# Kernel tuning notes

Hardware: AMD Instinct MI355X
Metric: run time of the kernel (lower is better)

## Reference

```python
import jax, jax.numpy as jnp
import numpy as np

B, S, HS = 2, 2048, 2048
H, KVH, D = 8, 1, 256
ROPE_BASE = 10000.0


def _rope_cos_sin(position_ids, dim, base=ROPE_BASE):
    # position_ids: (B, S) int -> cos/sin: (B, S, dim)
    inv_freq = 1.0 / (base ** (jnp.arange(0, dim, 2, dtype=jnp.float32) / dim))
    thetas = position_ids.astype(jnp.float32)[..., None] * inv_freq  # (B,S,dim/2)
    emb = jnp.concatenate([thetas, thetas], axis=-1)  # (B,S,dim)
    return jnp.cos(emb), jnp.sin(emb)


def _rotate_half(x):
    x1, x2 = jnp.split(x, 2, axis=-1)
    return jnp.concatenate([-x2, x1], axis=-1)


def _apply_rope(q, k, cos, sin):
    # q,k: (B,h,S,D); cos,sin: (B,S,D) -> unsqueeze head dim
    cos = cos[:, None, :, :]
    sin = sin[:, None, :, :]
    q_emb = q * cos + _rotate_half(q) * sin
    k_emb = k * cos + _rotate_half(k) * sin
    return q_emb, k_emb


def setup_inputs() -> dict:
    key = jax.random.key(0)
    k0, k1, k2, k3, k4 = jax.random.split(key, 5)
    hidden_states = jax.random.normal(k0, (B, S, HS), jnp.float32)
    # causal additive mask: 0 where j<=i, large negative otherwise
    causal = jnp.tril(jnp.ones((S, S), dtype=bool))
    attention_mask = jnp.where(causal, 0.0, -1e9).astype(jnp.float32)
    attention_mask = jnp.broadcast_to(attention_mask[None, None], (B, 1, S, S))
    position_ids = jnp.broadcast_to(jnp.arange(S, dtype=jnp.int32)[None], (B, S))
    scale = 0.02
    Wq = jax.random.normal(k1, (HS, H * D), jnp.float32) * scale
    Wk = jax.random.normal(k2, (HS, KVH * D), jnp.float32) * scale
    Wv = jax.random.normal(k3, (HS, KVH * D), jnp.float32) * scale
    Wo = jax.random.normal(k4, (H * D, HS), jnp.float32) * scale
    return {"hidden_states": hidden_states, "attention_mask": attention_mask,
            "position_ids": position_ids, "Wq": Wq, "Wk": Wk, "Wv": Wv, "Wo": Wo}


def reference(hidden_states, attention_mask, position_ids, Wq, Wk, Wv, Wo):
    bs, seq_len, _ = hidden_states.shape
    q = (hidden_states @ Wq).reshape(bs, seq_len, H, D).transpose(0, 2, 1, 3)     # (B,H,S,D)
    k = (hidden_states @ Wk).reshape(bs, seq_len, KVH, D).transpose(0, 2, 1, 3)   # (B,KVH,S,D)
    v = (hidden_states @ Wv).reshape(bs, seq_len, KVH, D).transpose(0, 2, 1, 3)
    cos, sin = _rope_cos_sin(position_ids, D)
    q, k = _apply_rope(q, k, cos, sin)
    n_rep = H // KVH
    k = jnp.repeat(k, n_rep, axis=1)  # GQA repeat -> (B,H,S,D)
    v = jnp.repeat(v, n_rep, axis=1)
    scores = jnp.einsum('bhqd,bhkd->bhqk', q, k) / jnp.sqrt(jnp.float32(D))
    scores = scores + attention_mask
    attn = jax.nn.softmax(scores.astype(jnp.float32), axis=-1).astype(q.dtype)
    out = jnp.einsum('bhqk,bhkd->bhqd', attn, v)            # (B,H,S,D)
    out = out.transpose(0, 2, 1, 3).reshape(bs, seq_len, H * D)
    return out @ Wo
```

## Files before the change

### kernel.cpp

```cpp
#include <hip/hip_runtime.h>
#include <hip/hip_bf16.h>

typedef __bf16 bf16x8 __attribute__((ext_vector_type(8)));
typedef __bf16 bf16x4 __attribute__((ext_vector_type(4)));
typedef float  f32x4  __attribute__((ext_vector_type(4)));

#define MFMA16(a, b, c) __builtin_amdgcn_mfma_f32_16x16x32_bf16((a), (b), (c), 0, 0, 0)

#define GLOBAL_AS(p) ((const __attribute__((address_space(1))) void*)(p))
#define LDS_AS(p)    ((__attribute__((address_space(3))) void*)(p))

static __device__ __forceinline__ void tr64(const float* __restrict__ W,
                                            __bf16* __restrict__ Bt,
                                            int K, int N, int n0, int k0,
                                            int tid, float (*t)[69])
{
    const int rk = tid >> 4, rc = (tid & 15) * 4;
#pragma unroll
    for (int p = 0; p < 4; ++p) {
        f32x4 v = *(const f32x4*)&W[(size_t)(k0 + p * 16 + rk) * N + n0 + rc];
        t[p * 16 + rk][rc + 0] = v[0];
        t[p * 16 + rk][rc + 1] = v[1];
        t[p * 16 + rk][rc + 2] = v[2];
        t[p * 16 + rk][rc + 3] = v[3];
    }
    __syncthreads();
    const int wn = tid >> 3, wk = (tid & 7) * 8;
#pragma unroll
    for (int p = 0; p < 2; ++p) {
        bf16x8 o;
#pragma unroll
        for (int j = 0; j < 8; ++j)
            o[j] = (__bf16)t[wk + j][p * 32 + wn];
        *(bf16x8*)&Bt[(size_t)(n0 + p * 32 + wn) * K + k0 + wk] = o;
    }
}

__global__ __launch_bounds__(256) void prep_kernel(const float* __restrict__ hidden,
                                                   __bf16* __restrict__ hb,
                                                   float2* __restrict__ cs,
                                                   const float* __restrict__ Wq,
                                                   const float* __restrict__ Wk,
                                                   const float* __restrict__ Wv,
                                                   const float* __restrict__ Wo,
                                                   __bf16* __restrict__ Wqkvt,
                                                   __bf16* __restrict__ Wot)
{
    __shared__ float tf[64][69];
    const int bx = blockIdx.x;
    const int tid = threadIdx.x;

    if (bx < 4096) {
        const int idx = bx * 256 + tid;
        const float4* p = (const float4*)hidden + (size_t)idx * 2;
        float4 a = p[0], b = p[1];
        bf16x8 o;
        o[0] = (__bf16)a.x; o[1] = (__bf16)a.y; o[2] = (__bf16)a.z; o[3] = (__bf16)a.w;
        o[4] = (__bf16)b.x; o[5] = (__bf16)b.y; o[6] = (__bf16)b.z; o[7] = (__bf16)b.w;
        ((bf16x8*)hb)[idx] = o;
    } else if (bx < 5120) {
        const int gid = (bx - 4096) * 256 + tid;
        const int s = gid >> 7, i = gid & 127;
        const float theta = (float)s * exp2f((float)i * (-13.287712379549449f / 128.f));
        float sn, c;
        sincosf(theta, &sn, &c);
        cs[s * 128 + i] = make_float2(c, sn);
    } else if (bx < 6144) {
        const int bidx = bx - 5120;
        tr64(Wq, Wqkvt, 2048, 2048, (bidx & 31) * 64, (bidx >> 5) * 64, tid, tf);
    } else if (bx < 6272) {
        const int bidx = bx - 6144;
        tr64(Wk, Wqkvt + (size_t)2048 * 2048, 2048, 256,
             (bidx & 3) * 64, (bidx >> 2) * 64, tid, tf);
    } else if (bx < 6400) {
        const int bidx = bx - 6272;
        tr64(Wv, Wqkvt + (size_t)2304 * 2048, 2048, 256,
             (bidx & 3) * 64, (bidx >> 2) * 64, tid, tf);
    } else {
        const int bidx = bx - 6400;
        tr64(Wo, Wot, 2048, 2048, (bidx & 31) * 64, (bidx >> 5) * 64, tid, tf);
    }
}

__global__ __launch_bounds__(256) void postq_kernel(__bf16* __restrict__ qkv,
                                                    const float2* __restrict__ cs,
                                                    __bf16* __restrict__ vT)
{
    __shared__ __bf16 tb[32][33];
    const int bx = blockIdx.x;
    const int t = threadIdx.x;

    if (bx < 4096) {
        const int bs = bx;
        const int s = bs & 2047;
        const float QS = 0.09016843787599907f;

        const int hh = t >> 5, i0 = (t & 31) * 4;
        float2 c0 = cs[s * 128 + i0 + 0], c1 = cs[s * 128 + i0 + 1];
        float2 c2 = cs[s * 128 + i0 + 2], c3 = cs[s * 128 + i0 + 3];
        {
            __bf16* p = qkv + (size_t)bs * 2560 + hh * 256 + i0;
            bf16x4 x1 = *(const bf16x4*)p;
            bf16x4 x2 = *(const bf16x4*)(p + 128);
            bf16x4 o1, o2;
            o1[0] = (__bf16)(((float)x1[0] * c0.x - (float)x2[0] * c0.y) * QS);
            o2[0] = (__bf16)(((float)x2[0] * c0.x + (float)x1[0] * c0.y) * QS);
            o1[1] = (__bf16)(((float)x1[1] * c1.x - (float)x2[1] * c1.y) * QS);
            o2[1] = (__bf16)(((float)x2[1] * c1.x + (float)x1[1] * c1.y) * QS);
            o1[2] = (__bf16)(((float)x1[2] * c2.x - (float)x2[2] * c2.y) * QS);
            o2[2] = (__bf16)(((float)x2[2] * c2.x + (float)x1[2] * c2.y) * QS);
            o1[3] = (__bf16)(((float)x1[3] * c3.x - (float)x2[3] * c3.y) * QS);
            o2[3] = (__bf16)(((float)x2[3] * c3.x + (float)x1[3] * c3.y) * QS);
            *(bf16x4*)p = o1;
            *(bf16x4*)(p + 128) = o2;
        }
        if (t < 32) {
            const int j0 = t * 4;
            float2 d0 = cs[s * 128 + j0 + 0], d1 = cs[s * 128 + j0 + 1];
            float2 d2 = cs[s * 128 + j0 + 2], d3 = cs[s * 128 + j0 + 3];
            __bf16* p = qkv + (size_t)bs * 2560 + 2048 + j0;
            bf16x4 x1 = *(const bf16x4*)p;
            bf16x4 x2 = *(const bf16x4*)(p + 128);
            bf16x4 o1, o2;
            o1[0] = (__bf16)((float)x1[0] * d0.x - (float)x2[0] * d0.y);
            o2[0] = (__bf16)((float)x2[0] * d0.x + (float)x1[0] * d0.y);
            o1[1] = (__bf16)((float)x1[1] * d1.x - (float)x2[1] * d1.y);
            o2[1] = (__bf16)((float)x2[1] * d1.x + (float)x1[1] * d1.y);
            o1[2] = (__bf16)((float)x1[2] * d2.x - (float)x2[2] * d2.y);
            o2[2] = (__bf16)((float)x2[2] * d2.x + (float)x1[2] * d2.y);
            o1[3] = (__bf16)((float)x1[3] * d3.x - (float)x2[3] * d3.y);
            o2[3] = (__bf16)((float)x2[3] * d3.x + (float)x1[3] * d3.y);
            *(bf16x4*)p = o1;
            *(bf16x4*)(p + 128) = o2;
        }
    } else {
        const int bidx = bx - 4096;
        const int s0 = (bidx & 63) * 32;
        const int d0 = ((bidx >> 6) & 7) * 32;
        const int b  = bidx >> 9;
        const int x = t & 31, y = t >> 5;
#pragma unroll
        for (int r = 0; r < 4; ++r)
            tb[y + r * 8][x] = qkv[(size_t)(b * 2048 + s0 + y + r * 8) * 2560 + 2304 + d0 + x];
        __syncthreads();
#pragma unroll
        for (int r = 0; r < 4; ++r)
            vT[(size_t)(b * 256 + d0 + y + r * 8) * 2048 + s0 + x] = tb[x][y + r * 8];
    }
}

template <typename TC>
__global__ __launch_bounds__(512, 2) void gemm_mp(const __bf16* __restrict__ A,
                                                  const __bf16* __restrict__ Bt,
                                                  TC* __restrict__ C,
                                                  int M, int N, int K)
{
    __shared__ __bf16 As[3][128 * 64];
    __shared__ __bf16 Bs[3][256 * 64];

    const int tid  = threadIdx.x;
    const int wave = tid >> 6, lane = tid & 63;
    const int quad = lane >> 4, l16 = lane & 15;
    const int wm = (wave >> 2) * 64, wn = (wave & 3) * 64;
    const int bm = blockIdx.y * 128, bn = blockIdx.x * 256;
    const int xk = l16 & 7;

    const int srow = tid >> 3;
    const int schk = (tid & 7) ^ (srow & 7);
    const __bf16* gA[2];
    const __bf16* gB[4];
#pragma unroll
    for (int p = 0; p < 2; ++p)
        gA[p] = A + (size_t)(bm + p * 64 + srow) * K + schk * 8;
#pragma unroll
    for (int p = 0; p < 4; ++p)
        gB[p] = Bt + (size_t)(bn + p * 64 + srow) * K + schk * 8;

#define STAGE_A2(s, t) do {                                                       \
    const size_t ko_ = (size_t)(t) * 64;                                          \
    __builtin_amdgcn_global_load_lds(GLOBAL_AS(gA[0] + ko_),                      \
        LDS_AS((char*)As[s] + tid * 16), 16, 0, 0);                               \
    __builtin_amdgcn_global_load_lds(GLOBAL_AS(gA[1] + ko_),                      \
        LDS_AS((char*)As[s] + 8192 + tid * 16), 16, 0, 0);                        \
} while (0)
#define STAGE_B01(s, t) do {                                                      \
    const size_t ko_ = (size_t)(t) * 64;                                          \
    __builtin_amdgcn_global_load_lds(GLOBAL_AS(gB[0] + ko_),                      \
        LDS_AS((char*)Bs[s] + tid * 16), 16, 0, 0);                               \
    __builtin_amdgcn_global_load_lds(GLOBAL_AS(gB[1] + ko_),                      \
        LDS_AS((char*)Bs[s] + 8192 + tid * 16), 16, 0, 0);                        \
} while (0)
#define STAGE_B23(s, t) do {                                                      \
    const size_t ko_ = (size_t)(t) * 64;                                          \
    __builtin_amdgcn_global_load_lds(GLOBAL_AS(gB[2] + ko_),                      \
        LDS_AS((char*)Bs[s] + 16384 + tid * 16), 16, 0, 0);                       \
    __builtin_amdgcn_global_load_lds(GLOBAL_AS(gB[3] + ko_),                      \
        LDS_AS((char*)Bs[s] + 24576 + tid * 16), 16, 0, 0);                       \
} while (0)

    f32x4 acc[4][4] = {};
    const int nk = K >> 6;

    STAGE_A2(0, 0); STAGE_B01(0, 0); STAGE_B23(0, 0);
    STAGE_A2(1, 1); STAGE_B01(1, 1); STAGE_B23(1, 1);
    asm volatile("s_waitcnt vmcnt(6)" ::: "memory");
    __builtin_amdgcn_s_barrier();

    int s = 0;
    for (int t = 0; t < nk; ++t) {
        const int sp = (s + 2 >= 3) ? s - 1 : s + 2;
        const bool more2 = (t + 2 < nk);
        const bool more1 = (t + 1 < nk);

        bf16x8 af[4][2], bfr[2][2];
#pragma unroll
        for (int mi = 0; mi < 4; ++mi)
#pragma unroll
            for (int kh = 0; kh < 2; ++kh)
                af[mi][kh] = *(const bf16x8*)
                    &As[s][(wm + mi * 16 + l16) * 64 + (((kh << 2) | quad) ^ xk) * 8];
#pragma unroll
        for (int ni = 0; ni < 2; ++ni)
#pragma unroll
            for (int kh = 0; kh < 2; ++kh)
                bfr[ni][kh] = *(const bf16x8*)
                    &Bs[s][(wn + ni * 16 + l16) * 64 + (((kh << 2) | quad) ^ xk) * 8];
        if (more2) { STAGE_A2(sp, t + 2); STAGE_B01(sp, t + 2); }
        __builtin_amdgcn_sched_barrier(0);
        __builtin_amdgcn_s_barrier();
        asm volatile("s_waitcnt lgkmcnt(0)" ::: "memory");
        __builtin_amdgcn_sched_barrier(0);
        __builtin_amdgcn_s_setprio(1);
#pragma unroll
        for (int ni = 0; ni < 2; ++ni)
#pragma unroll
            for (int mi = 0; mi < 4; ++mi) {
                acc[mi][ni] = MFMA16(af[mi][0], bfr[ni][0], acc[mi][ni]);
                acc[mi][ni] = MFMA16(af[mi][1], bfr[ni][1], acc[mi][ni]);
            }
        __builtin_amdgcn_s_setprio(0);
        __builtin_amdgcn_sched_barrier(0);
        __builtin_amdgcn_s_barrier();

        bf16x8 bf2[2][2];
#pragma unroll
        for (int ni = 0; ni < 2; ++ni)
#pragma unroll
            for (int kh = 0; kh < 2; ++kh)
                bf2[ni][kh] = *(const bf16x8*)
                    &Bs[s][(wn + (2 + ni) * 16 + l16) * 64 + (((kh << 2) | quad) ^ xk) * 8];
        if (more2) STAGE_B23(sp, t + 2);
        __builtin_amdgcn_sched_barrier(0);
        __builtin_amdgcn_s_barrier();
        asm volatile("s_waitcnt lgkmcnt(0)" ::: "memory");
        __builtin_amdgcn_sched_barrier(0);
        __builtin_amdgcn_s_setprio(1);
#pragma unroll
        for (int ni = 0; ni < 2; ++ni)
#pragma unroll
            for (int mi = 0; mi < 4; ++mi) {
                acc[mi][2 + ni] = MFMA16(af[mi][0], bf2[ni][0], acc[mi][2 + ni]);
                acc[mi][2 + ni] = MFMA16(af[mi][1], bf2[ni][1], acc[mi][2 + ni]);
            }
        __builtin_amdgcn_s_setprio(0);
        if (more1) {
            if (more2) asm volatile("s_waitcnt vmcnt(6)" ::: "memory");
            else       asm volatile("s_waitcnt vmcnt(0)" ::: "memory");
        }
        __builtin_amdgcn_sched_barrier(0);
        __builtin_amdgcn_s_barrier();
        s = (s + 1 == 3) ? 0 : s + 1;
    }
#undef STAGE_A2
#undef STAGE_B01
#undef STAGE_B23

#pragma unroll
    for (int mi = 0; mi < 4; ++mi)
#pragma unroll
        for (int ni = 0; ni < 4; ++ni)
#pragma unroll
            for (int r = 0; r < 4; ++r) {
                int row = bm + wm + mi * 16 + quad * 4 + r;
                int col = bn + wn + ni * 16 + l16;
                C[(size_t)row * N + col] = (TC)acc[mi][ni][r];
            }
}

static __device__ __forceinline__ void stage8(const __bf16* src, __bf16* dst,
                                              size_t src_step)
{
#pragma unroll
    for (int p = 0; p < 8; ++p)
        __builtin_amdgcn_global_load_lds(GLOBAL_AS(src + (size_t)p * src_step),
                                         LDS_AS(dst + p * 2048), 16, 0, 0);
}

__global__ __launch_bounds__(256, 2) void attn_kernel(const __bf16* __restrict__ qkv,
                                                      const __bf16* __restrict__ vTg,
                                                      __bf16* __restrict__ og)
{
    __shared__ __bf16 Ks[64 * 256];
    __shared__ __bf16 Vs[256 * 64];
    __shared__ __bf16 Ps[4][32][36];

    const int b = blockIdx.z, h = blockIdx.y;
    const int xx = (int)blockIdx.x;
    const int half = xx >> 1;
    const bool rev = ((xx & 1) == 0) ^ (b != 0);
    const int qt = rev ? 31 - half : half;
    const int q0 = qt * 64;
    const int tid  = threadIdx.x;
    const int wave = tid >> 6, lane = tid & 63;
    const int quad = lane >> 4, l16 = lane & 15;
    const int xork = l16 & 7;
    const int wm2 = wave >> 1, wn2 = wave & 1;

    bf16x8 onef;
#pragma unroll
    for (int e = 0; e < 8; ++e) onef[e] = (__bf16)1.0f;

    bf16x8 qf[2][8];
#pragma unroll
    for (int mi = 0; mi < 2; ++mi) {
        const __bf16* qptr = qkv + (size_t)(b * 2048 + q0 + wm2 * 32 + mi * 16 + l16) * 2560
                           + h * 256;
#pragma unroll
        for (int dc = 0; dc < 8; ++dc)
            qf[mi][dc] = *(const bf16x8*)(qptr + dc * 32 + quad * 8);
    }

    f32x4 oacc[2][16] = {};
    f32x4 lacc[2] = {};

    const int kKey0 = tid >> 5;
    const int kC    = (tid & 31) ^ (kKey0 & 7);
    const __bf16* kstage0 = qkv + (size_t)b * 2048 * 2560 + 2048
                          + (size_t)kKey0 * 2560 + kC * 8;
    const int vD0 = tid >> 3;
    const int vC  = (tid & 7) ^ (vD0 & 7);
    const __bf16* vstage0 = vTg + (size_t)b * 256 * 2048 + (size_t)vD0 * 2048 + vC * 8;
    __bf16* kdst = Ks + tid * 8;
    __bf16* vdst = Vs + tid * 8;

    int ckK[8];
#pragma unroll
    for (int dc = 0; dc < 8; ++dc) ckK[dc] = (dc * 4 + quad) ^ xork;
    const int chV = (wn2 * 4 + quad) ^ xork;

    stage8(kstage0, kdst, (size_t)8 * 2560);
    __builtin_amdgcn_sched_barrier(0);
    stage8(vstage0, vdst, (size_t)32 * 2048);
    __builtin_amdgcn_sched_barrier(0);

    for (int j0 = 0; j0 <= q0; j0 += 64) {
        const bool more = (j0 + 64 <= q0);

        asm volatile("s_waitcnt vmcnt(8)" ::: "memory");
        __builtin_amdgcn_s_barrier();
        __builtin_amdgcn_sched_barrier(0);

        f32x4 sc[2][2] = {};
        __builtin_amdgcn_s_setprio(1);
#pragma unroll
        for (int nt = 0; nt < 2; ++nt) {
            const __bf16* krow = &Ks[(wn2 * 32 + nt * 16 + l16) * 256];
#pragma unroll
            for (int dc = 0; dc < 8; ++dc) {
                bf16x8 kf = *(const bf16x8*)(krow + ckK[dc] * 8);
                sc[0][nt] = MFMA16(qf[0][dc], kf, sc[0][nt]);
                sc[1][nt] = MFMA16(qf[1][dc], kf, sc[1][nt]);
            }
        }
        __builtin_amdgcn_s_setprio(0);

        asm volatile("s_waitcnt lgkmcnt(0)" ::: "memory");
        __builtin_amdgcn_s_barrier();
        __builtin_amdgcn_sched_barrier(0);

        if (more) {
            stage8(kstage0 + (size_t)(j0 + 64) * 2560, kdst, (size_t)8 * 2560);
            __builtin_amdgcn_sched_barrier(0);
        }

        if (j0 == q0) {
#pragma unroll
            for (int nt = 0; nt < 2; ++nt) {
                int key = j0 + wn2 * 32 + nt * 16 + l16;
#pragma unroll
                for (int mi = 0; mi < 2; ++mi)
#pragma unroll
                    for (int r = 0; r < 4; ++r) {
                        int row = q0 + wm2 * 32 + mi * 16 + quad * 4 + r;
                        if (key > row) sc[mi][nt][r] = -1e30f;
                    }
            }
        }
#pragma unroll
        for (int mi = 0; mi < 2; ++mi)
#pragma unroll
            for (int nt = 0; nt < 2; ++nt)
#pragma unroll
                for (int r = 0; r < 4; ++r)
                    Ps[wave][mi * 16 + quad * 4 + r][nt * 16 + l16] =
                        (__bf16)exp2f(sc[mi][nt][r] - 8.f);
        bf16x8 pf0 = *(const bf16x8*)&Ps[wave][l16][quad * 8];
        bf16x8 pf1 = *(const bf16x8*)&Ps[wave][16 + l16][quad * 8];

        if (more) asm volatile("s_waitcnt vmcnt(8)" ::: "memory");
        else      asm volatile("s_waitcnt vmcnt(0)" ::: "memory");
        __builtin_amdgcn_s_barrier();
        __builtin_amdgcn_sched_barrier(0);

        __builtin_amdgcn_s_setprio(1);
#pragma unroll
        for (int dt = 0; dt < 16; ++dt) {
            const __bf16* vrow = &Vs[(dt * 16 + l16) * 64];
            bf16x8 vf = *(const bf16x8*)(vrow + chV * 8);
            oacc[0][dt] = MFMA16(pf0, vf, oacc[0][dt]);
            oacc[1][dt] = MFMA16(pf1, vf, oacc[1][dt]);
        }
        lacc[0] = MFMA16(pf0, onef, lacc[0]);
        lacc[1] = MFMA16(pf1, onef, lacc[1]);
        __builtin_amdgcn_s_setprio(0);

        asm volatile("s_waitcnt lgkmcnt(0)" ::: "memory");
        __builtin_amdgcn_s_barrier();
        __builtin_amdgcn_sched_barrier(0);

        if (more) {
            stage8(vstage0 + (j0 + 64), vdst, (size_t)32 * 2048);
            __builtin_amdgcn_sched_barrier(0);
        }
    }

    __syncthreads();
    float* oscr = (wm2 == 0) ? (float*)Ks : (float*)Vs;
    float* lscr = (float*)Ps;
    if (wn2 == 1) {
#pragma unroll
        for (int mi = 0; mi < 2; ++mi) {
#pragma unroll
            for (int dt = 0; dt < 16; ++dt)
#pragma unroll
                for (int r = 0; r < 4; ++r)
                    oscr[(mi * 16 + quad * 4 + r) * 256 + dt * 16 + l16] = oacc[mi][dt][r];
#pragma unroll
            for (int r = 0; r < 4; ++r)
                lscr[(wm2 * 32 + mi * 16 + quad * 4 + r) * 16 + l16] = lacc[mi][r];
        }
    }
    __syncthreads();
    if (wn2 == 0) {
#pragma unroll
        for (int mi = 0; mi < 2; ++mi) {
            float invl[4];
#pragma unroll
            for (int r = 0; r < 4; ++r)
                invl[r] = 1.f / (lacc[mi][r]
                        + lscr[(wm2 * 32 + mi * 16 + quad * 4 + r) * 16 + l16]);
#pragma unroll
            for (int dt = 0; dt < 16; ++dt)
#pragma unroll
                for (int r = 0; r < 4; ++r) {
                    float o = oacc[mi][dt][r]
                            + oscr[(mi * 16 + quad * 4 + r) * 256 + dt * 16 + l16];
                    int row = q0 + wm2 * 32 + mi * 16 + quad * 4 + r;
                    int col = h * 256 + dt * 16 + l16;
                    og[(size_t)(b * 2048 + row) * 2048 + col] = (__bf16)(o * invl[r]);
                }
        }
    }
}

extern "C" void kernel_launch(void* const* d_in, const int* in_sizes, int n_in,
                              void* d_out, int out_size, void* d_ws, size_t ws_size,
                              hipStream_t stream)
{
    (void)in_sizes; (void)n_in; (void)out_size; (void)ws_size;
    const float* hidden = (const float*)d_in[0];
    const float* Wq = (const float*)d_in[3];
    const float* Wk = (const float*)d_in[4];
    const float* Wv = (const float*)d_in[5];
    const float* Wo = (const float*)d_in[6];

    char* ws = (char*)d_ws;
    __bf16* hb    = (__bf16*)(ws);
    __bf16* qkv   = (__bf16*)(ws + (16u << 20));
    __bf16* vTb   = (__bf16*)(ws + (36u << 20));
    __bf16* ob    = (__bf16*)(ws + (38u << 20));
    __bf16* Wqkvt = (__bf16*)(ws + (54u << 20));
    __bf16* Wot   = (__bf16*)(ws + (64u << 20));
    float2* csb   = (float2*)(ws + (72u << 20));
    float* out = (float*)d_out;

    prep_kernel<<<dim3(7424), dim3(256), 0, stream>>>(hidden, hb, csb,
                                                      Wq, Wk, Wv, Wo, Wqkvt, Wot);
    gemm_mp<__bf16><<<dim3(10, 32), dim3(512), 0, stream>>>(hb, Wqkvt, qkv, 4096, 2560, 2048);
    postq_kernel<<<dim3(5120), dim3(256), 0, stream>>>(qkv, csb, vTb);
    attn_kernel<<<dim3(32, 8, 2), dim3(256), 0, stream>>>(qkv, vTb, ob);
    gemm_mp<float><<<dim3(8, 32), dim3(512), 0, stream>>>(ob, Wot, out, 4096, 2048, 2048);
}
```

Measured before the change: 338.8 us.

## Fuse RoPE, Q scaling and V transpose into QKV GEMM epilogue

Removes the separate postq kernel and applies RoPE plus the softmax scale to Q and K, and writes the transposed V, inside the QKV GEMM epilogue through an LDS scratch buffer. This saves a kernel launch and a full read-modify-write pass over the qkv buffer. The cost is extra LDS traffic and barriers in the epilogue, with half the waves idle during the RoPE store. The LDS is now declared as one raw array that the scratch buffer reuses.

```diff
diff --git a/kernel.cpp b/kernel.cpp
--- a/kernel.cpp
+++ b/kernel.cpp
@@ -82,81 +82,22 @@
     }
 }
 
-__global__ __launch_bounds__(256) void postq_kernel(__bf16* __restrict__ qkv,
-                                                    const float2* __restrict__ cs,
-                                                    __bf16* __restrict__ vT)
-{
-    __shared__ __bf16 tb[32][33];
-    const int bx = blockIdx.x;
-    const int t = threadIdx.x;
-
-    if (bx < 4096) {
-        const int bs = bx;
-        const int s = bs & 2047;
-        const float QS = 0.09016843787599907f;
-
-        const int hh = t >> 5, i0 = (t & 31) * 4;
-        float2 c0 = cs[s * 128 + i0 + 0], c1 = cs[s * 128 + i0 + 1];
-        float2 c2 = cs[s * 128 + i0 + 2], c3 = cs[s * 128 + i0 + 3];
-        {
-            __bf16* p = qkv + (size_t)bs * 2560 + hh * 256 + i0;
-            bf16x4 x1 = *(const bf16x4*)p;
-            bf16x4 x2 = *(const bf16x4*)(p + 128);
-            bf16x4 o1, o2;
-            o1[0] = (__bf16)(((float)x1[0] * c0.x - (float)x2[0] * c0.y) * QS);
-            o2[0] = (__bf16)(((float)x2[0] * c0.x + (float)x1[0] * c0.y) * QS);
-            o1[1] = (__bf16)(((float)x1[1] * c1.x - (float)x2[1] * c1.y) * QS);
-            o2[1] = (__bf16)(((float)x2[1] * c1.x + (float)x1[1] * c1.y) * QS);
-            o1[2] = (__bf16)(((float)x1[2] * c2.x - (float)x2[2] * c2.y) * QS);
-            o2[2] = (__bf16)(((float)x2[2] * c2.x + (float)x1[2] * c2.y) * QS);
-            o1[3] = (__bf16)(((float)x1[3] * c3.x - (float)x2[3] * c3.y) * QS);
-            o2[3] = (__bf16)(((float)x2[3] * c3.x + (float)x1[3] * c3.y) * QS);
-            *(bf16x4*)p = o1;
-            *(bf16x4*)(p + 128) = o2;
-        }
-        if (t < 32) {
-            const int j0 = t * 4;
-            float2 d0 = cs[s * 128 + j0 + 0], d1 = cs[s * 128 + j0 + 1];
-            float2 d2 = cs[s * 128 + j0 + 2], d3 = cs[s * 128 + j0 + 3];
-            __bf16* p = qkv + (size_t)bs * 2560 + 2048 + j0;
-            bf16x4 x1 = *(const bf16x4*)p;
-            bf16x4 x2 = *(const bf16x4*)(p + 128);
-            bf16x4 o1, o2;
-            o1[0] = (__bf16)((float)x1[0] * d0.x - (float)x2[0] * d0.y);
-            o2[0] = (__bf16)((float)x2[0] * d0.x + (float)x1[0] * d0.y);
-            o1[1] = (__bf16)((float)x1[1] * d1.x - (float)x2[1] * d1.y);
-            o2[1] = (__bf16)((float)x2[1] * d1.x + (float)x1[1] * d1.y);
-            o1[2] = (__bf16)((float)x1[2] * d2.x - (float)x2[2] * d2.y);
-            o2[2] = (__bf16)((float)x2[2] * d2.x + (float)x1[2] * d2.y);
-            o1[3] = (__bf16)((float)x1[3] * d3.x - (float)x2[3] * d3.y);
-            o2[3] = (__bf16)((float)x2[3] * d3.x + (float)x1[3] * d3.y);
-            *(bf16x4*)p = o1;
-            *(bf16x4*)(p + 128) = o2;
-        }
-    } else {
-        const int bidx = bx - 4096;
-        const int s0 = (bidx & 63) * 32;
-        const int d0 = ((bidx >> 6) & 7) * 32;
-        const int b  = bidx >> 9;
-        const int x = t & 31, y = t >> 5;
-#pragma unroll
-        for (int r = 0; r < 4; ++r)
-            tb[y + r * 8][x] = qkv[(size_t)(b * 2048 + s0 + y + r * 8) * 2560 + 2304 + d0 + x];
-        __syncthreads();
-#pragma unroll
-        for (int r = 0; r < 4; ++r)
-            vT[(size_t)(b * 256 + d0 + y + r * 8) * 2048 + s0 + x] = tb[x][y + r * 8];
-    }
-}
-
-template <typename TC>
+template <typename TC, int MODE>
 __global__ __launch_bounds__(512, 2) void gemm_mp(const __bf16* __restrict__ A,
                                                   const __bf16* __restrict__ Bt,
                                                   TC* __restrict__ C,
-                                                  int M, int N, int K)
+                                                  int M, int N, int K,
+                                                  const float2* __restrict__ cs,
+                                                  __bf16* __restrict__ vT)
 {
-    __shared__ __bf16 As[3][128 * 64];
-    __shared__ __bf16 Bs[3][256 * 64];
+    __shared__ __align__(16) char lds_raw[147456];
+    __bf16* Asp[3];
+    __bf16* Bsp[3];
+#pragma unroll
+    for (int i = 0; i < 3; ++i) {
+        Asp[i] = (__bf16*)(lds_raw + i * 16384);
+        Bsp[i] = (__bf16*)(lds_raw + 49152 + i * 32768);
+    }
 
     const int tid  = threadIdx.x;
     const int wave = tid >> 6, lane = tid & 63;
@@ -179,23 +120,23 @@
 #define STAGE_A2(s, t) do {                                                       \
     const size_t ko_ = (size_t)(t) * 64;                                          \
     __builtin_amdgcn_global_load_lds(GLOBAL_AS(gA[0] + ko_),                      \
-        LDS_AS((char*)As[s] + tid * 16), 16, 0, 0);                               \
+        LDS_AS((char*)Asp[s] + tid * 16), 16, 0, 0);                              \
     __builtin_amdgcn_global_load_lds(GLOBAL_AS(gA[1] + ko_),                      \
-        LDS_AS((char*)As[s] + 8192 + tid * 16), 16, 0, 0);                        \
+        LDS_AS((char*)Asp[s] + 8192 + tid * 16), 16, 0, 0);                       \
 } while (0)
 #define STAGE_B01(s, t) do {                                                      \
     const size_t ko_ = (size_t)(t) * 64;                                          \
     __builtin_amdgcn_global_load_lds(GLOBAL_AS(gB[0] + ko_),                      \
-        LDS_AS((char*)Bs[s] + tid * 16), 16, 0, 0);                               \
+        LDS_AS((char*)Bsp[s] + tid * 16), 16, 0, 0);                              \
     __builtin_amdgcn_global_load_lds(GLOBAL_AS(gB[1] + ko_),                      \
-        LDS_AS((char*)Bs[s] + 8192 + tid * 16), 16, 0, 0);                        \
+        LDS_AS((char*)Bsp[s] + 8192 + tid * 16), 16, 0, 0);                       \
 } while (0)
 #define STAGE_B23(s, t) do {                                                      \
     const size_t ko_ = (size_t)(t) * 64;                                          \
     __builtin_amdgcn_global_load_lds(GLOBAL_AS(gB[2] + ko_),                      \
-        LDS_AS((char*)Bs[s] + 16384 + tid * 16), 16, 0, 0);                       \
+        LDS_AS((char*)Bsp[s] + 16384 + tid * 16), 16, 0, 0);                      \
     __builtin_amdgcn_global_load_lds(GLOBAL_AS(gB[3] + ko_),                      \
-        LDS_AS((char*)Bs[s] + 24576 + tid * 16), 16, 0, 0);                       \
+        LDS_AS((char*)Bsp[s] + 24576 + tid * 16), 16, 0, 0);                      \
 } while (0)
 
     f32x4 acc[4][4] = {};
@@ -218,13 +159,13 @@
 #pragma unroll
             for (int kh = 0; kh < 2; ++kh)
                 af[mi][kh] = *(const bf16x8*)
-                    &As[s][(wm + mi * 16 + l16) * 64 + (((kh << 2) | quad) ^ xk) * 8];
+                    &Asp[s][(wm + mi * 16 + l16) * 64 + (((kh << 2) | quad) ^ xk) * 8];
 #pragma unroll
         for (int ni = 0; ni < 2; ++ni)
 #pragma unroll
             for (int kh = 0; kh < 2; ++kh)
                 bfr[ni][kh] = *(const bf16x8*)
-                    &Bs[s][(wn + ni * 16 + l16) * 64 + (((kh << 2) | quad) ^ xk) * 8];
+                    &Bsp[s][(wn + ni * 16 + l16) * 64 + (((kh << 2) | quad) ^ xk) * 8];
         if (more2) { STAGE_A2(sp, t + 2); STAGE_B01(sp, t + 2); }
         __builtin_amdgcn_sched_barrier(0);
         __builtin_amdgcn_s_barrier();
@@ -248,7 +189,7 @@
 #pragma unroll
             for (int kh = 0; kh < 2; ++kh)
                 bf2[ni][kh] = *(const bf16x8*)
-                    &Bs[s][(wn + (2 + ni) * 16 + l16) * 64 + (((kh << 2) | quad) ^ xk) * 8];
+                    &Bsp[s][(wn + (2 + ni) * 16 + l16) * 64 + (((kh << 2) | quad) ^ xk) * 8];
         if (more2) STAGE_B23(sp, t + 2);
         __builtin_amdgcn_sched_barrier(0);
         __builtin_amdgcn_s_barrier();
@@ -275,16 +216,83 @@
 #undef STAGE_B01
 #undef STAGE_B23
 
-#pragma unroll
-    for (int mi = 0; mi < 4; ++mi)
-#pragma unroll
-        for (int ni = 0; ni < 4; ++ni)
-#pragma unroll
-            for (int r = 0; r < 4; ++r) {
-                int row = bm + wm + mi * 16 + quad * 4 + r;
-                int col = bn + wn + ni * 16 + l16;
-                C[(size_t)row * N + col] = (TC)acc[mi][ni][r];
-            }
+    if constexpr (MODE == 0) {
+#pragma unroll
+        for (int mi = 0; mi < 4; ++mi)
+#pragma unroll
+            for (int ni = 0; ni < 4; ++ni)
+#pragma unroll
+                for (int r = 0; r < 4; ++r) {
+                    int row = bm + wm + mi * 16 + quad * 4 + r;
+                    int col = bn + wn + ni * 16 + l16;
+                    C[(size_t)row * N + col] = (TC)acc[mi][ni][r];
+                }
+    } else {
+        float* scr = (float*)lds_raw;
+        __syncthreads();
+        if (bn < 2304) {
+            if (wn >= 128) {
+#pragma unroll
+                for (int mi = 0; mi < 4; ++mi)
+#pragma unroll
+                    for (int ni = 0; ni < 4; ++ni)
+#pragma unroll
+                        for (int r = 0; r < 4; ++r) {
+                            int rl = wm + mi * 16 + quad * 4 + r;
+                            int i2 = (wn - 128) + ni * 16 + l16;
+                            scr[rl * 132 + i2] = acc[mi][ni][r];
+                        }
+            }
+            __syncthreads();
+            if (wn < 128) {
+                const float QS = 0.09016843787599907f;
+                const bool isq = (bn < 2048);
+#pragma unroll
+                for (int mi = 0; mi < 4; ++mi)
+#pragma unroll
+                    for (int ni = 0; ni < 4; ++ni)
+#pragma unroll
+                        for (int r = 0; r < 4; ++r) {
+                            int rl = wm + mi * 16 + quad * 4 + r;
+                            int i  = wn + ni * 16 + l16;
+                            int grow = bm + rl;
+                            int spos = grow & 2047;
+                            float2 c = cs[spos * 128 + i];
+                            float x1 = acc[mi][ni][r];
+                            float x2 = scr[rl * 132 + i];
+                            float o1 = x1 * c.x - x2 * c.y;
+                            float o2 = x2 * c.x + x1 * c.y;
+                            if (isq) { o1 *= QS; o2 *= QS; }
+                            C[(size_t)grow * N + bn + i]       = (TC)o1;
+                            C[(size_t)grow * N + bn + i + 128] = (TC)o2;
+                        }
+            }
+        } else {
+#pragma unroll
+            for (int mi = 0; mi < 4; ++mi)
+#pragma unroll
+                for (int ni = 0; ni < 4; ++ni)
+#pragma unroll
+                    for (int r = 0; r < 4; ++r) {
+                        int rl = wm + mi * 16 + quad * 4 + r;
+                        int d  = wn + ni * 16 + l16;
+                        scr[rl * 258 + d] = acc[mi][ni][r];
+                    }
+            __syncthreads();
+            const int d  = tid >> 1;
+            const int j0 = (tid & 1) * 64;
+            const int b  = bm >> 11;
+            const int sbase = bm & 2047;
+#pragma unroll
+            for (int c8 = 0; c8 < 8; ++c8) {
+                bf16x8 o;
+#pragma unroll
+                for (int e = 0; e < 8; ++e)
+                    o[e] = (__bf16)scr[(j0 + c8 * 8 + e) * 258 + d];
+                *(bf16x8*)&vT[((size_t)b * 256 + d) * 2048 + sbase + j0 + c8 * 8] = o;
+            }
+        }
+    }
 }
 
 static __device__ __forceinline__ void stage8(const __bf16* src, __bf16* dst,
@@ -496,8 +504,11 @@
 
     prep_kernel<<<dim3(7424), dim3(256), 0, stream>>>(hidden, hb, csb,
                                                       Wq, Wk, Wv, Wo, Wqkvt, Wot);
-    gemm_mp<__bf16><<<dim3(10, 32), dim3(512), 0, stream>>>(hb, Wqkvt, qkv, 4096, 2560, 2048);
-    postq_kernel<<<dim3(5120), dim3(256), 0, stream>>>(qkv, csb, vTb);
+    gemm_mp<__bf16, 1><<<dim3(10, 32), dim3(512), 0, stream>>>(hb, Wqkvt, qkv,
+                                                               4096, 2560, 2048,
+                                                               csb, vTb);
     attn_kernel<<<dim3(32, 8, 2), dim3(256), 0, stream>>>(qkv, vTb, ob);
-    gemm_mp<float><<<dim3(8, 32), dim3(512), 0, stream>>>(ob, Wot, out, 4096, 2048, 2048);
+    gemm_mp<float, 0><<<dim3(8, 32), dim3(512), 0, stream>>>(ob, Wot, out,
+                                                             4096, 2048, 2048,
+                                                             nullptr, nullptr);
 }
```

Measured after the change: 442.5 us. +30.6%, slower.
